# Kernel optimization log

Hardware: AMD Instinct MI355X
Metric: run time of the kernel (lower is better)

Reference implementation:

```python
import jax, jax.numpy as jnp
import numpy as np


def _gcn_norm(edge_index, edge_weight, n_nodes):
    # PyG gcn_norm with add_self_loops=True, fill_value=1.0.
    row, col = edge_index[0], edge_index[1]
    loop = jnp.arange(n_nodes, dtype=edge_index.dtype)
    row = jnp.concatenate([row, loop])
    col = jnp.concatenate([col, loop])
    w = jnp.concatenate([edge_weight, jnp.ones((n_nodes,), edge_weight.dtype)])
    deg = jax.ops.segment_sum(w, col, num_segments=n_nodes)
    dinv = jnp.where(deg > 0, jax.lax.rsqrt(deg), 0.0)
    norm = dinv[row] * w * dinv[col]
    return row, col, norm


def _gcn_conv(x, row, col, norm, W, b, n_nodes):
    h = x @ W                                  # [N, F_out]
    msg = h[row] * norm[:, None]               # gather + scale, [E+N, F_out]
    out = jax.ops.segment_sum(msg, col, num_segments=n_nodes)
    return out + b


def setup_inputs() -> dict:
    key = jax.random.key(0)
    k = jax.random.split(key, 7)
    N, E, Fin, Fout = 50000, 1600000, 256, 128
    H = 2 * Fout
    x = jax.random.normal(k[0], (N, Fin), dtype=jnp.float32)
    edge_index = jax.random.randint(k[1], (2, E), 0, N, dtype=jnp.int64)
    edge_weight = jax.random.uniform(k[2], (E,), dtype=jnp.float32)
    # Glorot init as in PyG GCNConv (weight stored as [in, out] here)
    s1 = float(np.sqrt(6.0 / (Fin + H)))
    s2 = float(np.sqrt(6.0 / (H + Fout)))
    W1 = jax.random.uniform(k[3], (Fin, H), minval=-s1, maxval=s1, dtype=jnp.float32)
    b1 = jnp.zeros((H,), jnp.float32)
    W2 = jax.random.uniform(k[4], (H, Fout), minval=-s2, maxval=s2, dtype=jnp.float32)
    b2 = jnp.zeros((Fout,), jnp.float32)
    return {"x": x, "edge_index": edge_index, "edge_weight": edge_weight,
            "W1": W1, "b1": b1, "W2": W2, "b2": b2}


def reference(x, edge_index, edge_weight, W1, b1, W2, b2):
    n_nodes = x.shape[0]
    # cached=True: normalization computed once, reused by both layers
    row, col, norm = _gcn_norm(edge_index, edge_weight, n_nodes)
    h = _gcn_conv(x, row, col, norm, W1, b1, n_nodes)
    h = jax.nn.relu(h)
    out = _gcn_conv(h, row, col, norm, W2, b2, n_nodes)
    return out
```

## Files before the change

### kernel.cpp

```cpp
#include <hip/hip_runtime.h>

typedef __attribute__((ext_vector_type(8))) short  short8;
typedef __attribute__((ext_vector_type(4))) float  f32x4;
typedef __attribute__((ext_vector_type(4))) ushort us4;
typedef __attribute__((ext_vector_type(4))) uint   u32x4;
typedef __attribute__((ext_vector_type(2))) uint   u32x2;

__device__ __forceinline__ float bf2f(ushort u) {
    union { uint i; float f; } c; c.i = ((uint)u) << 16; return c.f;
}
__device__ __forceinline__ float bits2f(uint b) {
    union { uint i; float f; } c; c.i = b; return c.f;
}
__device__ __forceinline__ ushort f2bf(float f) {
    union { float f; uint i; } c; c.f = f;
    uint b = c.i + 0x7fffu + ((c.i >> 16) & 1u);
    return (ushort)(b >> 16);
}

#define CMAX 96
#define CPK  (CMAX / 4)

__global__ void k_init64(unsigned long long* cur, int n) {
    int i = blockIdx.x * blockDim.x + threadIdx.x;
    if (i < n) cur[i] = 0ull;
}

__global__ void k_scatter1(const int* __restrict__ row, const int* __restrict__ col,
                           const float* __restrict__ w,
                           unsigned long long* __restrict__ cur,
                           uint* __restrict__ edgesP, int E) {
    int i = blockIdx.x * blockDim.x + threadIdx.x;
    if (i < E) {
        int r = row[i], c = col[i];
        float wv = w[i];
        unsigned long long inc = (1ull << 32) | (unsigned long long)(uint)(wv * 16777216.0f);
        unsigned long long old = atomicAdd(&cur[c], inc);
        uint slot = (uint)(old >> 32);
        if (slot < CMAX) {
            uint w16 = (uint)(wv * 65536.0f);
            if (w16 > 65535u) w16 = 65535u;
            edgesP[c * CMAX + (int)slot] = (w16 << 16) | (uint)(r & 0xffff);
        }
    }
}

__global__ void k_dinv2(const unsigned long long* __restrict__ cur,
                        float* __restrict__ dinv, int* __restrict__ cntp, int n) {
    int i = blockIdx.x * blockDim.x + threadIdx.x;
    if (i < n) {
        unsigned long long cc = cur[i];
        uint cnt = (uint)(cc >> 32);
        if (cnt > CMAX) cnt = CMAX;
        float wsum = (float)(uint)(cc & 0xffffffffull) * (1.0f / 16777216.0f);
        float deg = 1.0f + wsum;
        dinv[i] = rsqrtf(deg);
        cntp[i] = (int)((cnt + 3u) & ~3u);
    }
}

__global__ void k_normrw(const unsigned long long* __restrict__ cur,
                         uint* __restrict__ edgesP, const float* __restrict__ dinv, int N) {
    int tid = blockIdx.x * blockDim.x + threadIdx.x;
    if (tid >= N * CPK) return;
    int node = tid / CPK;
    int j0 = (tid - node * CPK) * 4;
    uint cnt = (uint)(cur[node] >> 32);
    if (cnt > CMAX) cnt = CMAX;
    int cp = (int)((cnt + 3u) & ~3u);
    if (j0 >= cp) return;
    float dc = dinv[node];
    int base = node * CMAX;
    #pragma unroll
    for (int j = j0; j < j0 + 4; ++j) {
        int idx = base + j;
        if (j < (int)cnt) {
            uint pk = edgesP[idx];
            uint r = pk & 0xffffu;
            float wv = (float)(pk >> 16) * (1.0f / 65536.0f);
            float nv = dinv[r] * wv * dc;
            edgesP[idx] = r | ((uint)f2bf(nv) << 16);
        } else if (j < cp) {
            edgesP[idx] = 0u;
        }
    }
}

__global__ void k_splitT(const float* __restrict__ W, ushort* __restrict__ Th,
                         ushort* __restrict__ Tl, int K, int N) {
    int i = blockIdx.x * 256 + threadIdx.x;
    if (i < K * N) {
        int k = i / N, n = i - k * N;
        float v = W[i];
        ushort hi = f2bf(v);
        ushort lo = f2bf(v - bf2f(hi));
        Th[(size_t)n * K + k] = hi;
        Tl[(size_t)n * K + k] = lo;
    }
}

#define LDA 40

__global__ __launch_bounds__(256)
void k_gemm3(const float* __restrict__ A, const ushort* __restrict__ BTh,
             const ushort* __restrict__ BTl, ushort* __restrict__ Cpan,
             int M, int Nc, int K) {
    __shared__ __align__(16) ushort As[2][128][LDA];
    __shared__ __align__(16) ushort Bs[2][128][LDA];

    const int t    = threadIdx.x;
    const int lane = t & 63;
    const int wid  = t >> 6;
    const int wm   = wid >> 1;
    const int wn   = wid & 1;
    const int ml   = lane & 15;
    const int kq   = lane >> 4;
    const int bm   = blockIdx.y * 128;
    const int bn   = blockIdx.x * 128;

    f32x4 acc[4][4];
    #pragma unroll
    for (int mt = 0; mt < 4; ++mt)
        #pragma unroll
        for (int nt = 0; nt < 4; ++nt) acc[mt][nt] = (f32x4){0.f, 0.f, 0.f, 0.f};

    for (int k0 = 0; k0 < K; k0 += 32) {
        #pragma unroll
        for (int it = 0; it < 4; ++it) {
            int idx = (t + it * 256) * 4;
            int r  = idx >> 5;
            int kk = idx & 31;
            int grow = bm + r;
            f32x4 v = (f32x4){0.f, 0.f, 0.f, 0.f};
            if (grow < M) v = *(const f32x4*)&A[(size_t)grow * K + k0 + kk];
            us4 hi, lo;
            #pragma unroll
            for (int j = 0; j < 4; ++j) {
                ushort h = f2bf(v[j]);
                hi[j] = h;
                lo[j] = f2bf(v[j] - bf2f(h));
            }
            *(us4*)&As[0][r][kk] = hi;
            *(us4*)&As[1][r][kk] = lo;
        }
        #pragma unroll
        for (int it = 0; it < 2; ++it) {
            int idx = (t + it * 256) * 8;
            int n  = idx >> 5;
            int kk = idx & 31;
            u32x4 vh = *(const u32x4*)&BTh[(size_t)(bn + n) * K + k0 + kk];
            *(u32x4*)&Bs[0][n][kk] = vh;
            u32x4 vl = *(const u32x4*)&BTl[(size_t)(bn + n) * K + k0 + kk];
            *(u32x4*)&Bs[1][n][kk] = vl;
        }
        __syncthreads();

        short8 a[4][2], b[4][2];
        #pragma unroll
        for (int mt = 0; mt < 4; ++mt) {
            a[mt][0] = *(const short8*)&As[0][wm * 64 + mt * 16 + ml][kq * 8];
            a[mt][1] = *(const short8*)&As[1][wm * 64 + mt * 16 + ml][kq * 8];
        }
        #pragma unroll
        for (int nt = 0; nt < 4; ++nt) {
            b[nt][0] = *(const short8*)&Bs[0][wn * 64 + nt * 16 + ml][kq * 8];
            b[nt][1] = *(const short8*)&Bs[1][wn * 64 + nt * 16 + ml][kq * 8];
        }
        #pragma unroll
        for (int mt = 0; mt < 4; ++mt)
            #pragma unroll
            for (int nt = 0; nt < 4; ++nt) {
                acc[mt][nt] = __builtin_amdgcn_mfma_f32_16x16x32_bf16(a[mt][0], b[nt][0], acc[mt][nt], 0, 0, 0);
                acc[mt][nt] = __builtin_amdgcn_mfma_f32_16x16x32_bf16(a[mt][0], b[nt][1], acc[mt][nt], 0, 0, 0);
                acc[mt][nt] = __builtin_amdgcn_mfma_f32_16x16x32_bf16(a[mt][1], b[nt][0], acc[mt][nt], 0, 0, 0);
            }
        __syncthreads();
    }

    #pragma unroll
    for (int mt = 0; mt < 4; ++mt) {
        int rbase = bm + wm * 64 + mt * 16 + kq * 4;
        #pragma unroll
        for (int nt = 0; nt < 4; ++nt) {
            int colg = bn + wn * 64 + nt * 16 + ml;
            size_t pbase = (size_t)(colg >> 5) * M * 32 + (colg & 31);
            #pragma unroll
            for (int r = 0; r < 4; ++r) {
                int rr = rbase + r;
                if (rr < M) Cpan[pbase + (size_t)rr * 32] = f2bf(acc[mt][nt][r]);
            }
        }
    }
}

#define NODES_PER_BLK 32

template <bool RELU>
__device__ __forceinline__
void aggr_body(const int* __restrict__ cntp, const uint* __restrict__ edges,
               const ushort* __restrict__ hpan, const float* __restrict__ dinv,
               const float* __restrict__ bias, float* __restrict__ out,
               int F, int npan, int N) {
    const int bid  = blockIdx.x;
    const int p    = bid % npan;
    const int wave = threadIdx.x >> 6;
    const int lane = threadIdx.x & 63;
    const int g    = lane >> 3;
    const int c    = lane & 7;
    const int node = (bid / npan) * NODES_PER_BLK + wave * 8 + g;
    const int fbase = p * 32 + c * 4;

    const ushort* hp = hpan + (size_t)p * N * 32 + c * 4;

    int beg = 0, end = 0;
    if (node < N) { beg = node * CMAX; end = beg + cntp[node]; }

    float a0 = 0.f, a1 = 0.f, a2 = 0.f, a3 = 0.f;
    int e = beg;
    u32x4 pk4 = (u32x4){0u, 0u, 0u, 0u};
    if (e < end) pk4 = *(const u32x4*)&edges[e];
    while (__any(e < end)) {
        u32x4 cur = pk4;
        int e2 = e + 4;
        if (e2 < end) pk4 = *(const u32x4*)&edges[e2];
        if (e < end) {
            #pragma unroll
            for (int j = 0; j < 4; ++j) {
                uint pk = cur[j];
                float nv = bits2f(pk & 0xffff0000u);
                int r = (int)(pk & 0xffffu);
                u32x2 hv = *(const u32x2*)(hp + (size_t)r * 32);
                a0 += nv * bits2f(hv[0] << 16);
                a1 += nv * bits2f(hv[0] & 0xffff0000u);
                a2 += nv * bits2f(hv[1] << 16);
                a3 += nv * bits2f(hv[1] & 0xffff0000u);
            }
        }
        e = e2;
    }

    if (node < N) {
        float di = dinv[node];
        float d2 = di * di;
        u32x2 hs = *(const u32x2*)(hp + (size_t)node * 32);
        f32x4 bv = *(const f32x4*)&bias[fbase];
        f32x4 v;
        v[0] = a0 + d2 * bits2f(hs[0] << 16)         + bv[0];
        v[1] = a1 + d2 * bits2f(hs[0] & 0xffff0000u) + bv[1];
        v[2] = a2 + d2 * bits2f(hs[1] << 16)         + bv[2];
        v[3] = a3 + d2 * bits2f(hs[1] & 0xffff0000u) + bv[3];
        if (RELU) {
            v[0] = fmaxf(v[0], 0.f); v[1] = fmaxf(v[1], 0.f);
            v[2] = fmaxf(v[2], 0.f); v[3] = fmaxf(v[3], 0.f);
        }
        *(f32x4*)&out[(size_t)node * F + fbase] = v;
    }
}

__global__ __launch_bounds__(256)
void k_aggr1(const int* __restrict__ cntp, const uint* __restrict__ edges,
             const ushort* __restrict__ hpan, const float* __restrict__ dinv,
             const float* __restrict__ bias, float* __restrict__ out,
             int F, int npan, int N) {
    aggr_body<true>(cntp, edges, hpan, dinv, bias, out, F, npan, N);
}

__global__ __launch_bounds__(256)
void k_aggr2(const int* __restrict__ cntp, const uint* __restrict__ edges,
             const ushort* __restrict__ hpan, const float* __restrict__ dinv,
             const float* __restrict__ bias, float* __restrict__ out,
             int F, int npan, int N) {
    aggr_body<false>(cntp, edges, hpan, dinv, bias, out, F, npan, N);
}


static inline char* bump(char*& p, size_t bytes) {
    char* r = p;
    p += (bytes + 255) & ~(size_t)255;
    return r;
}

extern "C" void kernel_launch(void* const* d_in, const int* in_sizes, int n_in,
                              void* d_out, int out_size, void* d_ws, size_t ws_size,
                              hipStream_t stream) {
    const float* x  = (const float*)d_in[0];
    const int*   ei = (const int*)d_in[1];
    const float* ew = (const float*)d_in[2];
    const float* W1 = (const float*)d_in[3];
    const float* b1 = (const float*)d_in[4];
    const float* W2 = (const float*)d_in[5];
    const float* b2 = (const float*)d_in[6];
    float* out = (float*)d_out;

    const int E    = in_sizes[2];
    const int H    = in_sizes[4];
    const int Fout = in_sizes[6];
    const int Fin  = in_sizes[3] / H;
    const int N    = in_sizes[0] / Fin;

    const int* row = ei;
    const int* col = ei + E;

    char* p = (char*)d_ws;
    float*  dinv   = (float*)bump(p, (size_t)N * 4);
    unsigned long long* cur64 = (unsigned long long*)bump(p, (size_t)N * 8);
    int*    cntp   = (int*)bump(p, (size_t)N * 4);
    uint*   edgesP = (uint*)bump(p, (size_t)N * CMAX * 4);
    ushort* WT1h   = (ushort*)bump(p, (size_t)Fin * H * 2);
    ushort* WT1l   = (ushort*)bump(p, (size_t)Fin * H * 2);
    ushort* WT2h   = (ushort*)bump(p, (size_t)H * Fout * 2);
    ushort* WT2l   = (ushort*)bump(p, (size_t)H * Fout * 2);
    ushort* h1     = (ushort*)bump(p, (size_t)N * H * 2);
    float*  a1     = (float*)bump(p, (size_t)N * H * 4);
    ushort* h2     = (ushort*)bump(p, (size_t)N * Fout * 2);

    k_init64<<<(N + 255) / 256, 256, 0, stream>>>(cur64, N);
    k_splitT<<<(Fin * H + 255) / 256, 256, 0, stream>>>(W1, WT1h, WT1l, Fin, H);
    k_splitT<<<(H * Fout + 255) / 256, 256, 0, stream>>>(W2, WT2h, WT2l, H, Fout);

    k_scatter1<<<(E + 255) / 256, 256, 0, stream>>>(row, col, ew, cur64, edgesP, E);
    k_dinv2<<<(N + 255) / 256, 256, 0, stream>>>(cur64, dinv, cntp, N);
    k_normrw<<<(N * CPK + 255) / 256, 256, 0, stream>>>(cur64, edgesP, dinv, N);

    const int chunks = (N + NODES_PER_BLK - 1) / NODES_PER_BLK;

    k_gemm3<<<dim3(H / 128, (N + 127) / 128), 256, 0, stream>>>(x, WT1h, WT1l, h1, N, H, Fin);
    k_aggr1<<<chunks * (H / 32), 256, 0, stream>>>(cntp, edgesP, h1, dinv, b1, a1, H, H / 32, N);

    k_gemm3<<<dim3(Fout / 128, (N + 127) / 128), 256, 0, stream>>>(a1, WT2h, WT2l, h2, N, Fout, H);
    k_aggr2<<<chunks * (Fout / 32), 256, 0, stream>>>(cntp, edgesP, h2, dinv, b2, out, Fout, Fout / 32, N);
}
```

Before: 449.9 us.

## Fuse first-layer GEMM and edge scatter into one launch; pad atomic counters

Merges the layer-1 GEMM and the edge-scatter/atomic counting kernel into a single grid, with block ranges chosen by block index. The compute-bound GEMM blocks and the atomic-bound scatter blocks can then run concurrently, and one launch boundary goes away. Each node's 64-bit counter is also padded to its own 64-byte slot so atomics on neighbouring nodes no longer share a cache line. In exchange, the counter array and its zeroing grow eightfold. The scatter blocks also allocate the GEMM's shared memory, which can reduce occupancy for those blocks.

```diff
diff --git a/kernel.cpp b/kernel.cpp
--- a/kernel.cpp
+++ b/kernel.cpp
@@ -21,35 +21,16 @@
 #define CMAX 96
 #define CPK  (CMAX / 4)
 
-__global__ void k_init64(unsigned long long* cur, int n) {
+__global__ void k_init64(uint* cur, int n16) {
     int i = blockIdx.x * blockDim.x + threadIdx.x;
-    if (i < n) cur[i] = 0ull;
-}
-
-__global__ void k_scatter1(const int* __restrict__ row, const int* __restrict__ col,
-                           const float* __restrict__ w,
-                           unsigned long long* __restrict__ cur,
-                           uint* __restrict__ edgesP, int E) {
-    int i = blockIdx.x * blockDim.x + threadIdx.x;
-    if (i < E) {
-        int r = row[i], c = col[i];
-        float wv = w[i];
-        unsigned long long inc = (1ull << 32) | (unsigned long long)(uint)(wv * 16777216.0f);
-        unsigned long long old = atomicAdd(&cur[c], inc);
-        uint slot = (uint)(old >> 32);
-        if (slot < CMAX) {
-            uint w16 = (uint)(wv * 65536.0f);
-            if (w16 > 65535u) w16 = 65535u;
-            edgesP[c * CMAX + (int)slot] = (w16 << 16) | (uint)(r & 0xffff);
-        }
-    }
+    if (i < n16) *(u32x4*)&cur[(size_t)i * 4] = (u32x4){0u, 0u, 0u, 0u};
 }
 
 __global__ void k_dinv2(const unsigned long long* __restrict__ cur,
                         float* __restrict__ dinv, int* __restrict__ cntp, int n) {
     int i = blockIdx.x * blockDim.x + threadIdx.x;
     if (i < n) {
-        unsigned long long cc = cur[i];
+        unsigned long long cc = cur[(size_t)i * 8];
         uint cnt = (uint)(cc >> 32);
         if (cnt > CMAX) cnt = CMAX;
         float wsum = (float)(uint)(cc & 0xffffffffull) * (1.0f / 16777216.0f);
@@ -65,7 +46,7 @@
     if (tid >= N * CPK) return;
     int node = tid / CPK;
     int j0 = (tid - node * CPK) * 4;
-    uint cnt = (uint)(cur[node] >> 32);
+    uint cnt = (uint)(cur[(size_t)node * 8] >> 32);
     if (cnt > CMAX) cnt = CMAX;
     int cp = (int)((cnt + 3u) & ~3u);
     if (j0 >= cp) return;
@@ -101,13 +82,11 @@
 
 #define LDA 40
 
-__global__ __launch_bounds__(256)
-void k_gemm3(const float* __restrict__ A, const ushort* __restrict__ BTh,
-             const ushort* __restrict__ BTl, ushort* __restrict__ Cpan,
-             int M, int Nc, int K) {
-    __shared__ __align__(16) ushort As[2][128][LDA];
-    __shared__ __align__(16) ushort Bs[2][128][LDA];
-
+__device__ __forceinline__
+void gemm3_body(const float* __restrict__ A, const ushort* __restrict__ BTh,
+                const ushort* __restrict__ BTl, ushort* __restrict__ Cpan,
+                int M, int Nc, int K, int bm, int bn,
+                ushort (*As)[128][LDA], ushort (*Bs)[128][LDA]) {
     const int t    = threadIdx.x;
     const int lane = t & 63;
     const int wid  = t >> 6;
@@ -115,8 +94,6 @@
     const int wn   = wid & 1;
     const int ml   = lane & 15;
     const int kq   = lane >> 4;
-    const int bm   = blockIdx.y * 128;
-    const int bn   = blockIdx.x * 128;
 
     f32x4 acc[4][4];
     #pragma unroll
@@ -191,6 +168,47 @@
             }
         }
     }
+}
+
+__global__ __launch_bounds__(256)
+void k_gemm3(const float* __restrict__ A, const ushort* __restrict__ BTh,
+             const ushort* __restrict__ BTl, ushort* __restrict__ Cpan,
+             int M, int Nc, int K) {
+    __shared__ __align__(16) ushort As[2][128][LDA];
+    __shared__ __align__(16) ushort Bs[2][128][LDA];
+    gemm3_body(A, BTh, BTl, Cpan, M, Nc, K, blockIdx.y * 128, blockIdx.x * 128, As, Bs);
+}
+
+__global__ __launch_bounds__(256)
+void k_fused1(const float* __restrict__ A, const ushort* __restrict__ BTh,
+              const ushort* __restrict__ BTl, ushort* __restrict__ Cpan,
+              int M, int Nc, int K, int gemmBlocks,
+              const int* __restrict__ row, const int* __restrict__ col,
+              const float* __restrict__ w,
+              unsigned long long* __restrict__ cur,
+              uint* __restrict__ edgesP, int E) {
+    __shared__ __align__(16) ushort As[2][128][LDA];
+    __shared__ __align__(16) ushort Bs[2][128][LDA];
+
+    const int bid = (int)blockIdx.x;
+    if (bid >= gemmBlocks) {
+        int i = (bid - gemmBlocks) * 256 + threadIdx.x;
+        if (i < E) {
+            int r = row[i], c = col[i];
+            float wv = w[i];
+            unsigned long long inc = (1ull << 32) | (unsigned long long)(uint)(wv * 16777216.0f);
+            unsigned long long old = atomicAdd(&cur[(size_t)c * 8], inc);
+            uint slot = (uint)(old >> 32);
+            if (slot < CMAX) {
+                uint w16 = (uint)(wv * 65536.0f);
+                if (w16 > 65535u) w16 = 65535u;
+                edgesP[c * CMAX + (int)slot] = (w16 << 16) | (uint)(r & 0xffff);
+            }
+        }
+        return;
+    }
+    const int nbn = Nc >> 7;
+    gemm3_body(A, BTh, BTl, Cpan, M, Nc, K, (bid / nbn) * 128, (bid % nbn) * 128, As, Bs);
 }
 
 #define NODES_PER_BLK 32
@@ -303,7 +321,7 @@
 
     char* p = (char*)d_ws;
     float*  dinv   = (float*)bump(p, (size_t)N * 4);
-    unsigned long long* cur64 = (unsigned long long*)bump(p, (size_t)N * 8);
+    unsigned long long* cur64 = (unsigned long long*)bump(p, (size_t)N * 64);
     int*    cntp   = (int*)bump(p, (size_t)N * 4);
     uint*   edgesP = (uint*)bump(p, (size_t)N * CMAX * 4);
     ushort* WT1h   = (ushort*)bump(p, (size_t)Fin * H * 2);
@@ -314,17 +332,21 @@
     float*  a1     = (float*)bump(p, (size_t)N * H * 4);
     ushort* h2     = (ushort*)bump(p, (size_t)N * Fout * 2);
 
-    k_init64<<<(N + 255) / 256, 256, 0, stream>>>(cur64, N);
+    const int n16 = N * 4;
+    k_init64<<<(n16 + 255) / 256, 256, 0, stream>>>((uint*)cur64, n16);
     k_splitT<<<(Fin * H + 255) / 256, 256, 0, stream>>>(W1, WT1h, WT1l, Fin, H);
     k_splitT<<<(H * Fout + 255) / 256, 256, 0, stream>>>(W2, WT2h, WT2l, H, Fout);
 
-    k_scatter1<<<(E + 255) / 256, 256, 0, stream>>>(row, col, ew, cur64, edgesP, E);
+    const int gb = (H / 128) * ((N + 127) / 128);
+    const int sb = (E + 255) / 256;
+    k_fused1<<<gb + sb, 256, 0, stream>>>(x, WT1h, WT1l, h1, N, H, Fin, gb,
+                                          row, col, ew, cur64, edgesP, E);
+
     k_dinv2<<<(N + 255) / 256, 256, 0, stream>>>(cur64, dinv, cntp, N);
     k_normrw<<<(N * CPK + 255) / 256, 256, 0, stream>>>(cur64, edgesP, dinv, N);
 
     const int chunks = (N + NODES_PER_BLK - 1) / NODES_PER_BLK;
 
-    k_gemm3<<<dim3(H / 128, (N + 127) / 128), 256, 0, stream>>>(x, WT1h, WT1l, h1, N, H, Fin);
     k_aggr1<<<chunks * (H / 32), 256, 0, stream>>>(cntp, edgesP, h1, dinv, b1, a1, H, H / 32, N);
 
     k_gemm3<<<dim3(Fout / 128, (N + 127) / 128), 256, 0, stream>>>(a1, WT2h, WT2l, h2, N, Fout, H);
```

New measurement: 406.8 us. 1.11x faster.

## Replace global-atomic CSR build with block-binned counting sort and fold dinv into GEMM

Applied to the files above, without the earlier changes.

Builds the per-destination edge lists with a two-level binned counting sort: a shared-memory histogram, a scan, binning into 64-node buckets, then per-bucket slot assignment using LDS atomics. This replaces one global 64-bit atomic per edge and removes the separate normalization rewrite pass. The source-side dinv is now applied in the GEMM epilogue, so edges store only the raw 16-bit weight and the destination dinv is applied once per node at the end of aggregation. The cost is several extra small kernels and a staging buffer aliased onto a1. Edge order within a node and the rounding of the pre-scaled bf16 features also change.

```diff
diff --git a/kernel.cpp b/kernel.cpp
--- a/kernel.cpp
+++ b/kernel.cpp
@@ -18,70 +18,117 @@
     return (ushort)(b >> 16);
 }
 
-#define CMAX 96
-#define CPK  (CMAX / 4)
-
-__global__ void k_init64(unsigned long long* cur, int n) {
-    int i = blockIdx.x * blockDim.x + threadIdx.x;
-    if (i < n) cur[i] = 0ull;
-}
-
-__global__ void k_scatter1(const int* __restrict__ row, const int* __restrict__ col,
-                           const float* __restrict__ w,
-                           unsigned long long* __restrict__ cur,
-                           uint* __restrict__ edgesP, int E) {
-    int i = blockIdx.x * blockDim.x + threadIdx.x;
-    if (i < E) {
-        int r = row[i], c = col[i];
+#define CMAX  96
+#define NBLK  256
+#define NBMAX 1024
+
+__global__ void k_histA(const int* __restrict__ col, int* __restrict__ counts,
+                        int E, int NB) {
+    __shared__ uint hist[NBMAX];
+    for (int j = threadIdx.x; j < NB; j += 256) hist[j] = 0u;
+    __syncthreads();
+    for (int i = blockIdx.x * 256 + threadIdx.x; i < E; i += 256 * NBLK)
+        atomicAdd(&hist[((uint)col[i]) >> 6], 1u);
+    __syncthreads();
+    for (int j = threadIdx.x; j < NB; j += 256)
+        counts[j * NBLK + blockIdx.x] = (int)hist[j];
+}
+
+__global__ void k_scanB1(int* __restrict__ counts, int* __restrict__ btot) {
+    __shared__ int s[256];
+    int b = blockIdx.x, t = threadIdx.x;
+    int v = counts[b * NBLK + t];
+    s[t] = v; __syncthreads();
+    for (int off = 1; off < 256; off <<= 1) {
+        int x = (t >= off) ? s[t - off] : 0;
+        __syncthreads();
+        s[t] += x;
+        __syncthreads();
+    }
+    counts[b * NBLK + t] = s[t] - v;
+    if (t == 255) btot[b] = s[255];
+}
+
+__global__ void k_scanB2(const int* __restrict__ btot, int* __restrict__ bbase, int NB) {
+    __shared__ int s[256];
+    int t = threadIdx.x;
+    int v[4]; int sum = 0;
+    #pragma unroll
+    for (int j = 0; j < 4; ++j) {
+        int i = t * 4 + j;
+        v[j] = (i < NB) ? btot[i] : 0;
+        sum += v[j];
+    }
+    s[t] = sum; __syncthreads();
+    for (int off = 1; off < 256; off <<= 1) {
+        int x = (t >= off) ? s[t - off] : 0;
+        __syncthreads();
+        s[t] += x;
+        __syncthreads();
+    }
+    int excl = s[t] - sum;
+    #pragma unroll
+    for (int j = 0; j < 4; ++j) {
+        int i = t * 4 + j;
+        if (i <= NB) bbase[i] = excl;
+        excl += v[j];
+    }
+}
+
+__global__ void k_binC(const int* __restrict__ row, const int* __restrict__ col,
+                       const float* __restrict__ w,
+                       const int* __restrict__ counts, const int* __restrict__ bbase,
+                       unsigned long long* __restrict__ recs, int E, int NB) {
+    __shared__ uint cur[NBMAX];
+    for (int j = threadIdx.x; j < NB; j += 256)
+        cur[j] = (uint)(bbase[j] + counts[j * NBLK + blockIdx.x]);
+    __syncthreads();
+    for (int i = blockIdx.x * 256 + threadIdx.x; i < E; i += 256 * NBLK) {
+        int c = col[i], r = row[i];
         float wv = w[i];
-        unsigned long long inc = (1ull << 32) | (unsigned long long)(uint)(wv * 16777216.0f);
-        unsigned long long old = atomicAdd(&cur[c], inc);
-        uint slot = (uint)(old >> 32);
-        if (slot < CMAX) {
-            uint w16 = (uint)(wv * 65536.0f);
-            if (w16 > 65535u) w16 = 65535u;
-            edgesP[c * CMAX + (int)slot] = (w16 << 16) | (uint)(r & 0xffff);
-        }
-    }
-}
-
-__global__ void k_dinv2(const unsigned long long* __restrict__ cur,
-                        float* __restrict__ dinv, int* __restrict__ cntp, int n) {
-    int i = blockIdx.x * blockDim.x + threadIdx.x;
-    if (i < n) {
-        unsigned long long cc = cur[i];
-        uint cnt = (uint)(cc >> 32);
-        if (cnt > CMAX) cnt = CMAX;
-        float wsum = (float)(uint)(cc & 0xffffffffull) * (1.0f / 16777216.0f);
-        float deg = 1.0f + wsum;
-        dinv[i] = rsqrtf(deg);
-        cntp[i] = (int)((cnt + 3u) & ~3u);
-    }
-}
-
-__global__ void k_normrw(const unsigned long long* __restrict__ cur,
-                         uint* __restrict__ edgesP, const float* __restrict__ dinv, int N) {
-    int tid = blockIdx.x * blockDim.x + threadIdx.x;
-    if (tid >= N * CPK) return;
-    int node = tid / CPK;
-    int j0 = (tid - node * CPK) * 4;
-    uint cnt = (uint)(cur[node] >> 32);
-    if (cnt > CMAX) cnt = CMAX;
-    int cp = (int)((cnt + 3u) & ~3u);
-    if (j0 >= cp) return;
-    float dc = dinv[node];
-    int base = node * CMAX;
-    #pragma unroll
-    for (int j = j0; j < j0 + 4; ++j) {
-        int idx = base + j;
-        if (j < (int)cnt) {
-            uint pk = edgesP[idx];
-            uint r = pk & 0xffffu;
-            float wv = (float)(pk >> 16) * (1.0f / 65536.0f);
-            float nv = dinv[r] * wv * dc;
-            edgesP[idx] = r | ((uint)f2bf(nv) << 16);
-        } else if (j < cp) {
-            edgesP[idx] = 0u;
+        uint w16 = (uint)(wv * 65536.0f);
+        if (w16 > 65535u) w16 = 65535u;
+        uint b = ((uint)c) >> 6;
+        uint pos = atomicAdd(&cur[b], 1u);
+        recs[pos] = ((unsigned long long)(uint)c << 32)
+                  | (unsigned long long)((w16 << 16) | (uint)(r & 0xffff));
+    }
+}
+
+__global__ void k_binD(const unsigned long long* __restrict__ recs,
+                       const int* __restrict__ bbase,
+                       uint* __restrict__ edgesP, int* __restrict__ cntp,
+                       float* __restrict__ dinv, int N, int NB) {
+    __shared__ uint cnt[64], ws[64], cur2[64];
+    int b = blockIdx.x, t = threadIdx.x;
+    if (t < 64) { cnt[t] = 0u; ws[t] = 0u; cur2[t] = 0u; }
+    __syncthreads();
+    int lo = bbase[b], hi = bbase[b + 1];
+    for (int i = lo + t; i < hi; i += 256) {
+        unsigned long long rec = recs[i];
+        uint cl = ((uint)(rec >> 32)) & 63u;
+        atomicAdd(&cnt[cl], 1u);
+        atomicAdd(&ws[cl], (uint)((rec >> 16) & 0xffffu));
+    }
+    __syncthreads();
+    for (int i = lo + t; i < hi; i += 256) {
+        unsigned long long rec = recs[i];
+        uint cg = (uint)(rec >> 32);
+        uint slot = atomicAdd(&cur2[cg & 63u], 1u);
+        if (slot < CMAX) edgesP[(size_t)cg * CMAX + slot] = (uint)rec;
+    }
+    __syncthreads();
+    if (t < 64) {
+        int node = b * 64 + t;
+        if (node < N) {
+            uint c0 = cnt[t];
+            if (c0 > CMAX) c0 = CMAX;
+            int cp = (int)((c0 + 3u) & ~3u);
+            for (int j = (int)c0; j < cp; ++j)
+                edgesP[(size_t)node * CMAX + j] = 0u;
+            float deg = 1.0f + (float)ws[t] * (1.0f / 65536.0f);
+            dinv[node] = rsqrtf(deg);
+            cntp[node] = cp;
         }
     }
 }
@@ -104,7 +151,7 @@
 __global__ __launch_bounds__(256)
 void k_gemm3(const float* __restrict__ A, const ushort* __restrict__ BTh,
              const ushort* __restrict__ BTl, ushort* __restrict__ Cpan,
-             int M, int Nc, int K) {
+             const float* __restrict__ dinv, int M, int Nc, int K) {
     __shared__ __align__(16) ushort As[2][128][LDA];
     __shared__ __align__(16) ushort Bs[2][128][LDA];
 
@@ -187,7 +234,7 @@
             #pragma unroll
             for (int r = 0; r < 4; ++r) {
                 int rr = rbase + r;
-                if (rr < M) Cpan[pbase + (size_t)rr * 32] = f2bf(acc[mt][nt][r]);
+                if (rr < M) Cpan[pbase + (size_t)rr * 32] = f2bf(acc[mt][nt][r] * dinv[rr]);
             }
         }
     }
@@ -227,7 +274,7 @@
             #pragma unroll
             for (int j = 0; j < 4; ++j) {
                 uint pk = cur[j];
-                float nv = bits2f(pk & 0xffff0000u);
+                float nv = (float)(pk >> 16);
                 int r = (int)(pk & 0xffffu);
                 u32x2 hv = *(const u32x2*)(hp + (size_t)r * 32);
                 a0 += nv * bits2f(hv[0] << 16);
@@ -240,15 +287,15 @@
     }
 
     if (node < N) {
-        float di = dinv[node];
-        float d2 = di * di;
+        float dc = dinv[node];
+        float sc = dc * (1.0f / 65536.0f);
         u32x2 hs = *(const u32x2*)(hp + (size_t)node * 32);
         f32x4 bv = *(const f32x4*)&bias[fbase];
         f32x4 v;
-        v[0] = a0 + d2 * bits2f(hs[0] << 16)         + bv[0];
-        v[1] = a1 + d2 * bits2f(hs[0] & 0xffff0000u) + bv[1];
-        v[2] = a2 + d2 * bits2f(hs[1] << 16)         + bv[2];
-        v[3] = a3 + d2 * bits2f(hs[1] & 0xffff0000u) + bv[3];
+        v[0] = fmaf(sc, a0, fmaf(dc, bits2f(hs[0] << 16),         bv[0]));
+        v[1] = fmaf(sc, a1, fmaf(dc, bits2f(hs[0] & 0xffff0000u), bv[1]));
+        v[2] = fmaf(sc, a2, fmaf(dc, bits2f(hs[1] << 16),         bv[2]));
+        v[3] = fmaf(sc, a3, fmaf(dc, bits2f(hs[1] & 0xffff0000u), bv[3]));
         if (RELU) {
             v[0] = fmaxf(v[0], 0.f); v[1] = fmaxf(v[1], 0.f);
             v[2] = fmaxf(v[2], 0.f); v[3] = fmaxf(v[3], 0.f);
@@ -297,15 +344,18 @@
     const int Fout = in_sizes[6];
     const int Fin  = in_sizes[3] / H;
     const int N    = in_sizes[0] / Fin;
+    const int NB   = (N + 63) >> 6;
 
     const int* row = ei;
     const int* col = ei + E;
 
     char* p = (char*)d_ws;
     float*  dinv   = (float*)bump(p, (size_t)N * 4);
-    unsigned long long* cur64 = (unsigned long long*)bump(p, (size_t)N * 8);
     int*    cntp   = (int*)bump(p, (size_t)N * 4);
     uint*   edgesP = (uint*)bump(p, (size_t)N * CMAX * 4);
+    int*    counts = (int*)bump(p, (size_t)NBMAX * NBLK * 4);
+    int*    btot   = (int*)bump(p, (size_t)NBMAX * 4);
+    int*    bbase  = (int*)bump(p, (size_t)(NBMAX + 1) * 4);
     ushort* WT1h   = (ushort*)bump(p, (size_t)Fin * H * 2);
     ushort* WT1l   = (ushort*)bump(p, (size_t)Fin * H * 2);
     ushort* WT2h   = (ushort*)bump(p, (size_t)H * Fout * 2);
@@ -314,19 +364,22 @@
     float*  a1     = (float*)bump(p, (size_t)N * H * 4);
     ushort* h2     = (ushort*)bump(p, (size_t)N * Fout * 2);
 
-    k_init64<<<(N + 255) / 256, 256, 0, stream>>>(cur64, N);
+    unsigned long long* recs = (unsigned long long*)a1;
+
     k_splitT<<<(Fin * H + 255) / 256, 256, 0, stream>>>(W1, WT1h, WT1l, Fin, H);
     k_splitT<<<(H * Fout + 255) / 256, 256, 0, stream>>>(W2, WT2h, WT2l, H, Fout);
 
-    k_scatter1<<<(E + 255) / 256, 256, 0, stream>>>(row, col, ew, cur64, edgesP, E);
-    k_dinv2<<<(N + 255) / 256, 256, 0, stream>>>(cur64, dinv, cntp, N);
-    k_normrw<<<(N * CPK + 255) / 256, 256, 0, stream>>>(cur64, edgesP, dinv, N);
+    k_histA<<<NBLK, 256, 0, stream>>>(col, counts, E, NB);
+    k_scanB1<<<NB, 256, 0, stream>>>(counts, btot);
+    k_scanB2<<<1, 256, 0, stream>>>(btot, bbase, NB);
+    k_binC<<<NBLK, 256, 0, stream>>>(row, col, ew, counts, bbase, recs, E, NB);
+    k_binD<<<NB, 256, 0, stream>>>(recs, bbase, edgesP, cntp, dinv, N, NB);
 
     const int chunks = (N + NODES_PER_BLK - 1) / NODES_PER_BLK;
 
-    k_gemm3<<<dim3(H / 128, (N + 127) / 128), 256, 0, stream>>>(x, WT1h, WT1l, h1, N, H, Fin);
+    k_gemm3<<<dim3(H / 128, (N + 127) / 128), 256, 0, stream>>>(x, WT1h, WT1l, h1, dinv, N, H, Fin);
     k_aggr1<<<chunks * (H / 32), 256, 0, stream>>>(cntp, edgesP, h1, dinv, b1, a1, H, H / 32, N);
 
-    k_gemm3<<<dim3(Fout / 128, (N + 127) / 128), 256, 0, stream>>>(a1, WT2h, WT2l, h2, N, Fout, H);
+    k_gemm3<<<dim3(Fout / 128, (N + 127) / 128), 256, 0, stream>>>(a1, WT2h, WT2l, h2, dinv, N, Fout, H);
     k_aggr2<<<chunks * (Fout / 32), 256, 0, stream>>>(cntp, edgesP, h2, dinv, b2, out, Fout, Fout / 32, N);
 }
```

After: 419.6 us. 6.7% less time.
